# Performance work log

Measured on AMD Instinct MI355X. Metric: run time of the kernel, lower is better.

## Reference

```python
import jax, jax.numpy as jnp
import numpy as np

DELTA = 0.1
B, U_DIM, D_DIM, H_DIM, Y_DIM = 4096, 256, 64, 8192, 256
ORDER = H_DIM // 2  # 2x2 rotation blocks


def setup_inputs() -> dict:
    key = jax.random.key(0)
    k = jax.random.split(key, 6)
    u = jax.random.normal(k[0], (B, U_DIM), jnp.float32)
    du = jax.random.normal(k[1], (B, D_DIM), jnp.float32)
    h = jax.random.normal(k[2], (1, H_DIM), jnp.float32)          # h_init state
    # torch.nn.init.uniform_ -> U[0,1); +0.05 keeps 1/omega well-conditioned
    omega = jax.random.uniform(k[3], (ORDER,), jnp.float32) + 0.05
    B_w = jax.random.normal(k[4], (H_DIM, U_DIM + D_DIM), jnp.float32) / np.sqrt(U_DIM + D_DIM)
    C_w = jax.random.normal(k[5], (Y_DIM, H_DIM), jnp.float32) / np.sqrt(H_DIM)
    return {"u": u, "du": du, "h": h, "omega": omega, "B_w": B_w, "C_w": C_w}


def reference(u, du, h, omega, B_w, C_w):
    cos_t = jnp.cos(omega * DELTA)   # [order]
    sin_t = jnp.sin(omega * DELTA)   # [order]
    # exact rotation of state pairs: h viewed as [*, order, 2]
    hp = h.reshape(-1, ORDER, 2)
    h1 = cos_t * hp[..., 0] + sin_t * hp[..., 1]
    h2 = -sin_t * hp[..., 0] + cos_t * hp[..., 1]
    rec = jnp.stack([h1, h2], axis=-1).reshape(h.shape[0], -1)    # [1, h_dim]
    # input projection u_hat = B([du, u])
    udu = jnp.concatenate([du, u], axis=1)                        # [B, d+u]
    u_hat = (udu @ B_w.T).reshape(-1, ORDER, 2)                   # [B, order, 2]
    cm1 = cos_t - 1.0
    inp1 = (sin_t * u_hat[..., 0] - cm1 * u_hat[..., 1]) / omega
    inp2 = (cm1 * u_hat[..., 0] + sin_t * u_hat[..., 1]) / omega
    inp = jnp.stack([inp1, inp2], axis=-1).reshape(udu.shape[0], -1)  # [B, h_dim]
    h_new = rec + inp                                             # broadcast [B, h_dim]
    # sigma = identity, C linear readout (no bias)
    y = h_new @ C_w.T                                             # [B, y_dim]
    return y
```

## Files before the change

### kernel.cpp

```cpp
#include <hip/hip_runtime.h>
#include <hip/hip_bf16.h>

#define BN    4096
#define U_DIM 256
#define D_DIM 64
#define H_DIM 8192
#define Y_DIM 256
#define C_DIM 320
#define DELTAF 0.1f

typedef __bf16 bf16_t;
typedef __attribute__((ext_vector_type(8))) bf16_t bf16x8;
typedef __attribute__((ext_vector_type(4))) float f32x4;

__global__ __launch_bounds__(256) void gemm_E(
    const float* __restrict__ Cw, const float* __restrict__ Bw,
    const float* __restrict__ omega, const float* __restrict__ hin,
    float* __restrict__ E, float* __restrict__ y0) {
  const int b = blockIdx.x;
  const int t = threadIdx.x;
  const int wave = t >> 6, lane = t & 63;
  const int wm = wave >> 1, wn = wave & 1;
  const int l15 = lane & 15, quad = lane >> 4;

  __shared__ bf16_t lA[2][64][72];
  __shared__ bf16_t lB[2][64][72];
  __shared__ __align__(16) float cS[352], cC[352], cI[352];

  const int p = (b * 20) >> 8;
  const int bs = (256 * p + 19) / 20;
  const int P = (256 * (p + 1) + 19) / 20 - bs;
  const int c = b - bs;
  const int it0 = (c * 128) / P;
  const int it1 = ((c + 1) * 128) / P;
  const int k0 = it0 * 64;
  const int niter = it1 - it0;
  const int bm = p / 5, bn = p % 5;

  const int npairs = niter * 32;
  for (int j = t; j < npairs; j += 256) {
    const float om = omega[(k0 >> 1) + j];
    const float ang = om * DELTAF;
    cS[j] = __sinf(ang);
    cC[j] = __cosf(ang) - 1.0f;
    cI[j] = 1.0f / om;
  }
  __syncthreads();

  const int ar = t >> 2, ak = (t & 3) * 16;
  const float* gA = Cw + (size_t)(bm * 64 + ar) * H_DIM + ak;
  const float* gBb = Bw + (size_t)bn * 64 + lane;

  float4 va[4], hv[4];
  float bv[16];
  float y0acc = 0.f;

  auto gload = [&](int kk) {
#pragma unroll
    for (int q = 0; q < 4; ++q)
      va[q] = *(const float4*)(gA + kk + q * 4);
    const float* pb = gBb + (size_t)(kk + wave * 16) * C_DIM;
#pragma unroll
    for (int j = 0; j < 16; ++j) bv[j] = pb[(size_t)j * C_DIM];
    if (bn == 0) {
#pragma unroll
      for (int q = 0; q < 4; ++q)
        hv[q] = *(const float4*)(hin + kk + ak + q * 4);
    }
  };
  auto stage = [&](int kk, int buf) {
    const int jp = ((kk - k0) >> 1) + (ak >> 1);
#pragma unroll
    for (int h = 0; h < 2; ++h) {
      const float4 cs = *(const float4*)&cS[jp + h * 4];
      const float4 cc = *(const float4*)&cC[jp + h * 4];
      const float4 ci = *(const float4*)&cI[jp + h * 4];
      const float4 v0 = va[2 * h], v1 = va[2 * h + 1];
      union {
        bf16_t x[8];
        int4 v;
      } pa;
      pa.x[0] = (bf16_t)((v0.x * cs.x + v0.y * cc.x) * ci.x);
      pa.x[1] = (bf16_t)((v0.y * cs.x - v0.x * cc.x) * ci.x);
      pa.x[2] = (bf16_t)((v0.z * cs.y + v0.w * cc.y) * ci.y);
      pa.x[3] = (bf16_t)((v0.w * cs.y - v0.z * cc.y) * ci.y);
      pa.x[4] = (bf16_t)((v1.x * cs.z + v1.y * cc.z) * ci.z);
      pa.x[5] = (bf16_t)((v1.y * cs.z - v1.x * cc.z) * ci.z);
      pa.x[6] = (bf16_t)((v1.z * cs.w + v1.w * cc.w) * ci.w);
      pa.x[7] = (bf16_t)((v1.w * cs.w - v1.z * cc.w) * ci.w);
      *(int4*)&lA[buf][ar][ak + h * 8] = pa.v;
      if (bn == 0) {
        const float4 h0 = hv[2 * h], h1 = hv[2 * h + 1];
        const float c0 = cc.x + 1.f, c1 = cc.y + 1.f;
        const float c2 = cc.z + 1.f, c3 = cc.w + 1.f;
        y0acc += v0.x * (c0 * h0.x + cs.x * h0.y) +
                 v0.y * (c0 * h0.y - cs.x * h0.x) +
                 v0.z * (c1 * h0.z + cs.y * h0.w) +
                 v0.w * (c1 * h0.w - cs.y * h0.z) +
                 v1.x * (c2 * h1.x + cs.z * h1.y) +
                 v1.y * (c2 * h1.y - cs.z * h1.x) +
                 v1.z * (c3 * h1.z + cs.w * h1.w) +
                 v1.w * (c3 * h1.w - cs.w * h1.z);
      }
    }
#pragma unroll
    for (int h = 0; h < 2; ++h) {
      union {
        bf16_t x[8];
        int4 v;
      } pb;
#pragma unroll
      for (int j = 0; j < 8; ++j) pb.x[j] = (bf16_t)bv[h * 8 + j];
      *(int4*)&lB[buf][lane][wave * 16 + h * 8] = pb.v;
    }
  };

  f32x4 acc[2][2] = {};
  gload(k0);
  stage(k0, 0);
  if (niter > 1) gload(k0 + 64);
#pragma unroll 1
  for (int i = 0; i < niter; ++i) {
    __syncthreads();
    const int cur = i & 1;
#pragma unroll
    for (int kq = 0; kq < 2; ++kq) {
      const bf16x8 a0 = *(bf16x8*)&lA[cur][wm * 32 + l15][kq * 32 + quad * 8];
      const bf16x8 a1 = *(bf16x8*)&lA[cur][wm * 32 + 16 + l15][kq * 32 + quad * 8];
      const bf16x8 b0 = *(bf16x8*)&lB[cur][wn * 32 + l15][kq * 32 + quad * 8];
      const bf16x8 b1 = *(bf16x8*)&lB[cur][wn * 32 + 16 + l15][kq * 32 + quad * 8];
      acc[0][0] = __builtin_amdgcn_mfma_f32_16x16x32_bf16(a0, b0, acc[0][0], 0, 0, 0);
      acc[0][1] = __builtin_amdgcn_mfma_f32_16x16x32_bf16(a0, b1, acc[0][1], 0, 0, 0);
      acc[1][0] = __builtin_amdgcn_mfma_f32_16x16x32_bf16(a1, b0, acc[1][0], 0, 0, 0);
      acc[1][1] = __builtin_amdgcn_mfma_f32_16x16x32_bf16(a1, b1, acc[1][1], 0, 0, 0);
    }
    if (i + 1 < niter) {
      stage(k0 + (i + 1) * 64, cur ^ 1);
      if (i + 2 < niter) gload(k0 + (i + 2) * 64);
    }
  }

#pragma unroll
  for (int mt = 0; mt < 2; ++mt)
#pragma unroll
    for (int nt = 0; nt < 2; ++nt) {
      const int col = bn * 64 + wn * 32 + nt * 16 + l15;
#pragma unroll
      for (int r = 0; r < 4; ++r) {
        const int row = bm * 64 + wm * 32 + mt * 16 + quad * 4 + r;
        atomicAdd(&E[row * C_DIM + col], acc[mt][nt][r]);
      }
    }
  if (bn == 0) {
    y0acc += __shfl_xor(y0acc, 1);
    y0acc += __shfl_xor(y0acc, 2);
    if ((t & 3) == 0) atomicAdd(&y0[bm * 64 + ar], y0acc);
  }
}

__global__ __launch_bounds__(256) void gemm_Y(
    const float* __restrict__ u, const float* __restrict__ du,
    const float* __restrict__ E, const float* __restrict__ y0,
    float* __restrict__ out) {
  const int bm = blockIdx.x;
  const int bn = blockIdx.y;
  const int t = threadIdx.x;
  const int wave = t >> 6, lane = t & 63;
  const int wm = wave >> 1, wn = wave & 1;
  const int l15 = lane & 15, quad = lane >> 4;

  __shared__ bf16_t lA[2][64][72];
  __shared__ bf16_t lB[2][64][72];

  const int ar = t >> 2;
  const int ak = (t & 3) * 16;

  float4 va[4], ve[4];
  auto gload = [&](int kk) {
    const int col = kk + ak;
    const float* p = (col < D_DIM)
                         ? du + (size_t)(bm * 64 + ar) * D_DIM + col
                         : u + (size_t)(bm * 64 + ar) * U_DIM + (col - D_DIM);
#pragma unroll
    for (int q = 0; q < 4; ++q) va[q] = *(const float4*)(p + q * 4);
    const float* pe = E + (size_t)(bn * 64 + ar) * C_DIM + col;
#pragma unroll
    for (int q = 0; q < 4; ++q) ve[q] = *(const float4*)(pe + q * 4);
  };
  auto stage = [&](int buf) {
#pragma unroll
    for (int h = 0; h < 2; ++h) {
      union {
        bf16_t x[8];
        int4 v;
      } pa, pb;
      const float4 a0 = va[2 * h], a1 = va[2 * h + 1];
      const float4 e0 = ve[2 * h], e1 = ve[2 * h + 1];
      pa.x[0] = (bf16_t)a0.x; pa.x[1] = (bf16_t)a0.y;
      pa.x[2] = (bf16_t)a0.z; pa.x[3] = (bf16_t)a0.w;
      pa.x[4] = (bf16_t)a1.x; pa.x[5] = (bf16_t)a1.y;
      pa.x[6] = (bf16_t)a1.z; pa.x[7] = (bf16_t)a1.w;
      pb.x[0] = (bf16_t)e0.x; pb.x[1] = (bf16_t)e0.y;
      pb.x[2] = (bf16_t)e0.z; pb.x[3] = (bf16_t)e0.w;
      pb.x[4] = (bf16_t)e1.x; pb.x[5] = (bf16_t)e1.y;
      pb.x[6] = (bf16_t)e1.z; pb.x[7] = (bf16_t)e1.w;
      *(int4*)&lA[buf][ar][ak + h * 8] = pa.v;
      *(int4*)&lB[buf][ar][ak + h * 8] = pb.v;
    }
  };

  f32x4 acc[2][2] = {};
  gload(0);
  stage(0);
  gload(64);
#pragma unroll
  for (int i = 0; i < 5; ++i) {
    __syncthreads();
    const int cur = i & 1;
#pragma unroll
    for (int kq = 0; kq < 2; ++kq) {
      const bf16x8 a0 = *(bf16x8*)&lA[cur][wm * 32 + l15][kq * 32 + quad * 8];
      const bf16x8 a1 = *(bf16x8*)&lA[cur][wm * 32 + 16 + l15][kq * 32 + quad * 8];
      const bf16x8 b0 = *(bf16x8*)&lB[cur][wn * 32 + l15][kq * 32 + quad * 8];
      const bf16x8 b1 = *(bf16x8*)&lB[cur][wn * 32 + 16 + l15][kq * 32 + quad * 8];
      acc[0][0] = __builtin_amdgcn_mfma_f32_16x16x32_bf16(a0, b0, acc[0][0], 0, 0, 0);
      acc[0][1] = __builtin_amdgcn_mfma_f32_16x16x32_bf16(a0, b1, acc[0][1], 0, 0, 0);
      acc[1][0] = __builtin_amdgcn_mfma_f32_16x16x32_bf16(a1, b0, acc[1][0], 0, 0, 0);
      acc[1][1] = __builtin_amdgcn_mfma_f32_16x16x32_bf16(a1, b1, acc[1][1], 0, 0, 0);
    }
    if (i < 4) {
      stage(cur ^ 1);
      if (i < 3) gload((i + 2) * 64);
    }
  }
#pragma unroll
  for (int nt = 0; nt < 2; ++nt) {
    const int col = bn * 64 + wn * 32 + nt * 16 + l15;
    const float yc = y0[col];
#pragma unroll
    for (int mt = 0; mt < 2; ++mt) {
#pragma unroll
      for (int r = 0; r < 4; ++r) {
        const int row = bm * 64 + wm * 32 + mt * 16 + quad * 4 + r;
        out[(size_t)row * Y_DIM + col] = acc[mt][nt][r] + yc;
      }
    }
  }
}

extern "C" void kernel_launch(void* const* d_in, const int* in_sizes, int n_in,
                              void* d_out, int out_size, void* d_ws,
                              size_t ws_size, hipStream_t stream) {
  const float* u = (const float*)d_in[0];
  const float* du = (const float*)d_in[1];
  const float* hin = (const float*)d_in[2];
  const float* omega = (const float*)d_in[3];
  const float* Bw = (const float*)d_in[4];
  const float* Cw = (const float*)d_in[5];
  float* out = (float*)d_out;

  char* ws = (char*)d_ws;
  float* E = (float*)ws;
  float* y0 = (float*)(ws + 327680);

  gemm_E<<<256, 256, 0, stream>>>(Cw, Bw, omega, hin, E, y0);
  gemm_Y<<<dim3(BN / 64, Y_DIM / 64), 256, 0, stream>>>(u, du, E, y0, out);
}
```

Baseline: 93.89 us.

## Double K-tile in gemm_E and load all of K upfront in gemm_Y

gemm_E now uses 128-wide K tiles instead of 64, halving the per-block iteration count and the barriers, with larger shared buffers and register staging. gemm_Y drops its double-buffered K loop: each block loads the full 320-deep K slice of inputs and E into shared memory at once, syncs once, then runs all MFMAs. Both kernels get launch_bounds(256,1), letting the compiler use more registers. The cost is more LDS and register use per block, which can reduce occupancy and leaves no overlap between loads and compute in gemm_Y.

```diff
diff --git a/kernel.cpp b/kernel.cpp
--- a/kernel.cpp
+++ b/kernel.cpp
@@ -13,7 +13,7 @@
 typedef __attribute__((ext_vector_type(8))) bf16_t bf16x8;
 typedef __attribute__((ext_vector_type(4))) float f32x4;
 
-__global__ __launch_bounds__(256) void gemm_E(
+__global__ __launch_bounds__(256, 1) void gemm_E(
     const float* __restrict__ Cw, const float* __restrict__ Bw,
     const float* __restrict__ omega, const float* __restrict__ hin,
     float* __restrict__ E, float* __restrict__ y0) {
@@ -23,21 +23,21 @@
   const int wm = wave >> 1, wn = wave & 1;
   const int l15 = lane & 15, quad = lane >> 4;
 
-  __shared__ bf16_t lA[2][64][72];
-  __shared__ bf16_t lB[2][64][72];
-  __shared__ __align__(16) float cS[352], cC[352], cI[352];
+  __shared__ bf16_t lA[2][64][136];
+  __shared__ bf16_t lB[2][64][136];
+  __shared__ __align__(16) float cS[384], cC[384], cI[384];
 
   const int p = (b * 20) >> 8;
   const int bs = (256 * p + 19) / 20;
   const int P = (256 * (p + 1) + 19) / 20 - bs;
   const int c = b - bs;
-  const int it0 = (c * 128) / P;
-  const int it1 = ((c + 1) * 128) / P;
-  const int k0 = it0 * 64;
+  const int it0 = (c * 64) / P;
+  const int it1 = ((c + 1) * 64) / P;
+  const int k0 = it0 * 128;
   const int niter = it1 - it0;
   const int bm = p / 5, bn = p % 5;
 
-  const int npairs = niter * 32;
+  const int npairs = niter * 64;
   for (int j = t; j < npairs; j += 256) {
     const float om = omega[(k0 >> 1) + j];
     const float ang = om * DELTAF;
@@ -47,31 +47,31 @@
   }
   __syncthreads();
 
-  const int ar = t >> 2, ak = (t & 3) * 16;
+  const int ar = t >> 2, ak = (t & 3) * 32;
   const float* gA = Cw + (size_t)(bm * 64 + ar) * H_DIM + ak;
   const float* gBb = Bw + (size_t)bn * 64 + lane;
 
-  float4 va[4], hv[4];
-  float bv[16];
+  float4 va[8], hv[8];
+  float bv[32];
   float y0acc = 0.f;
 
   auto gload = [&](int kk) {
 #pragma unroll
-    for (int q = 0; q < 4; ++q)
+    for (int q = 0; q < 8; ++q)
       va[q] = *(const float4*)(gA + kk + q * 4);
-    const float* pb = gBb + (size_t)(kk + wave * 16) * C_DIM;
-#pragma unroll
-    for (int j = 0; j < 16; ++j) bv[j] = pb[(size_t)j * C_DIM];
+    const float* pb = gBb + (size_t)(kk + wave * 32) * C_DIM;
+#pragma unroll
+    for (int j = 0; j < 32; ++j) bv[j] = pb[(size_t)j * C_DIM];
     if (bn == 0) {
 #pragma unroll
-      for (int q = 0; q < 4; ++q)
+      for (int q = 0; q < 8; ++q)
         hv[q] = *(const float4*)(hin + kk + ak + q * 4);
     }
   };
   auto stage = [&](int kk, int buf) {
     const int jp = ((kk - k0) >> 1) + (ak >> 1);
 #pragma unroll
-    for (int h = 0; h < 2; ++h) {
+    for (int h = 0; h < 4; ++h) {
       const float4 cs = *(const float4*)&cS[jp + h * 4];
       const float4 cc = *(const float4*)&cC[jp + h * 4];
       const float4 ci = *(const float4*)&cI[jp + h * 4];
@@ -104,27 +104,27 @@
       }
     }
 #pragma unroll
-    for (int h = 0; h < 2; ++h) {
+    for (int h = 0; h < 4; ++h) {
       union {
         bf16_t x[8];
         int4 v;
       } pb;
 #pragma unroll
       for (int j = 0; j < 8; ++j) pb.x[j] = (bf16_t)bv[h * 8 + j];
-      *(int4*)&lB[buf][lane][wave * 16 + h * 8] = pb.v;
+      *(int4*)&lB[buf][lane][wave * 32 + h * 8] = pb.v;
     }
   };
 
   f32x4 acc[2][2] = {};
   gload(k0);
   stage(k0, 0);
-  if (niter > 1) gload(k0 + 64);
+  if (niter > 1) gload(k0 + 128);
 #pragma unroll 1
   for (int i = 0; i < niter; ++i) {
     __syncthreads();
     const int cur = i & 1;
 #pragma unroll
-    for (int kq = 0; kq < 2; ++kq) {
+    for (int kq = 0; kq < 4; ++kq) {
       const bf16x8 a0 = *(bf16x8*)&lA[cur][wm * 32 + l15][kq * 32 + quad * 8];
       const bf16x8 a1 = *(bf16x8*)&lA[cur][wm * 32 + 16 + l15][kq * 32 + quad * 8];
       const bf16x8 b0 = *(bf16x8*)&lB[cur][wn * 32 + l15][kq * 32 + quad * 8];
@@ -135,8 +135,8 @@
       acc[1][1] = __builtin_amdgcn_mfma_f32_16x16x32_bf16(a1, b1, acc[1][1], 0, 0, 0);
     }
     if (i + 1 < niter) {
-      stage(k0 + (i + 1) * 64, cur ^ 1);
-      if (i + 2 < niter) gload(k0 + (i + 2) * 64);
+      stage(k0 + (i + 1) * 128, cur ^ 1);
+      if (i + 2 < niter) gload(k0 + (i + 2) * 128);
     }
   }
 
@@ -158,7 +158,7 @@
   }
 }
 
-__global__ __launch_bounds__(256) void gemm_Y(
+__global__ __launch_bounds__(256, 1) void gemm_Y(
     const float* __restrict__ u, const float* __restrict__ du,
     const float* __restrict__ E, const float* __restrict__ y0,
     float* __restrict__ out) {
@@ -169,33 +169,40 @@
   const int wm = wave >> 1, wn = wave & 1;
   const int l15 = lane & 15, quad = lane >> 4;
 
-  __shared__ bf16_t lA[2][64][72];
-  __shared__ bf16_t lB[2][64][72];
+  __shared__ bf16_t lA[64][328];
+  __shared__ bf16_t lB[64][328];
 
   const int ar = t >> 2;
   const int ak = (t & 3) * 16;
 
-  float4 va[4], ve[4];
-  auto gload = [&](int kk) {
-    const int col = kk + ak;
-    const float* p = (col < D_DIM)
-                         ? du + (size_t)(bm * 64 + ar) * D_DIM + col
-                         : u + (size_t)(bm * 64 + ar) * U_DIM + (col - D_DIM);
-#pragma unroll
-    for (int q = 0; q < 4; ++q) va[q] = *(const float4*)(p + q * 4);
-    const float* pe = E + (size_t)(bn * 64 + ar) * C_DIM + col;
-#pragma unroll
-    for (int q = 0; q < 4; ++q) ve[q] = *(const float4*)(pe + q * 4);
-  };
-  auto stage = [&](int buf) {
+  float4 va[20], ve[20];
+  {
+    const float* pd = du + (size_t)(bm * 64 + ar) * D_DIM + ak;
+#pragma unroll
+    for (int q = 0; q < 4; ++q) va[q] = *(const float4*)(pd + q * 4);
+    const float* pu = u + (size_t)(bm * 64 + ar) * U_DIM + ak;
+#pragma unroll
+    for (int ck = 1; ck < 5; ++ck)
+#pragma unroll
+      for (int q = 0; q < 4; ++q)
+        va[4 * ck + q] = *(const float4*)(pu + (ck - 1) * 64 + q * 4);
+    const float* pe = E + (size_t)(bn * 64 + ar) * C_DIM + ak;
+#pragma unroll
+    for (int ck = 0; ck < 5; ++ck)
+#pragma unroll
+      for (int q = 0; q < 4; ++q)
+        ve[4 * ck + q] = *(const float4*)(pe + ck * 64 + q * 4);
+  }
+#pragma unroll
+  for (int ck = 0; ck < 5; ++ck) {
 #pragma unroll
     for (int h = 0; h < 2; ++h) {
       union {
         bf16_t x[8];
         int4 v;
       } pa, pb;
-      const float4 a0 = va[2 * h], a1 = va[2 * h + 1];
-      const float4 e0 = ve[2 * h], e1 = ve[2 * h + 1];
+      const float4 a0 = va[4 * ck + 2 * h], a1 = va[4 * ck + 2 * h + 1];
+      const float4 e0 = ve[4 * ck + 2 * h], e1 = ve[4 * ck + 2 * h + 1];
       pa.x[0] = (bf16_t)a0.x; pa.x[1] = (bf16_t)a0.y;
       pa.x[2] = (bf16_t)a0.z; pa.x[3] = (bf16_t)a0.w;
       pa.x[4] = (bf16_t)a1.x; pa.x[5] = (bf16_t)a1.y;
@@ -204,34 +211,23 @@
       pb.x[2] = (bf16_t)e0.z; pb.x[3] = (bf16_t)e0.w;
       pb.x[4] = (bf16_t)e1.x; pb.x[5] = (bf16_t)e1.y;
       pb.x[6] = (bf16_t)e1.z; pb.x[7] = (bf16_t)e1.w;
-      *(int4*)&lA[buf][ar][ak + h * 8] = pa.v;
-      *(int4*)&lB[buf][ar][ak + h * 8] = pb.v;
-    }
-  };
+      *(int4*)&lA[ar][ck * 64 + ak + h * 8] = pa.v;
+      *(int4*)&lB[ar][ck * 64 + ak + h * 8] = pb.v;
+    }
+  }
+  __syncthreads();
 
   f32x4 acc[2][2] = {};
-  gload(0);
-  stage(0);
-  gload(64);
-#pragma unroll
-  for (int i = 0; i < 5; ++i) {
-    __syncthreads();
-    const int cur = i & 1;
-#pragma unroll
-    for (int kq = 0; kq < 2; ++kq) {
-      const bf16x8 a0 = *(bf16x8*)&lA[cur][wm * 32 + l15][kq * 32 + quad * 8];
-      const bf16x8 a1 = *(bf16x8*)&lA[cur][wm * 32 + 16 + l15][kq * 32 + quad * 8];
-      const bf16x8 b0 = *(bf16x8*)&lB[cur][wn * 32 + l15][kq * 32 + quad * 8];
-      const bf16x8 b1 = *(bf16x8*)&lB[cur][wn * 32 + 16 + l15][kq * 32 + quad * 8];
-      acc[0][0] = __builtin_amdgcn_mfma_f32_16x16x32_bf16(a0, b0, acc[0][0], 0, 0, 0);
-      acc[0][1] = __builtin_amdgcn_mfma_f32_16x16x32_bf16(a0, b1, acc[0][1], 0, 0, 0);
-      acc[1][0] = __builtin_amdgcn_mfma_f32_16x16x32_bf16(a1, b0, acc[1][0], 0, 0, 0);
-      acc[1][1] = __builtin_amdgcn_mfma_f32_16x16x32_bf16(a1, b1, acc[1][1], 0, 0, 0);
-    }
-    if (i < 4) {
-      stage(cur ^ 1);
-      if (i < 3) gload((i + 2) * 64);
-    }
+#pragma unroll
+  for (int ks = 0; ks < 10; ++ks) {
+    const bf16x8 a0 = *(bf16x8*)&lA[wm * 32 + l15][ks * 32 + quad * 8];
+    const bf16x8 a1 = *(bf16x8*)&lA[wm * 32 + 16 + l15][ks * 32 + quad * 8];
+    const bf16x8 b0 = *(bf16x8*)&lB[wn * 32 + l15][ks * 32 + quad * 8];
+    const bf16x8 b1 = *(bf16x8*)&lB[wn * 32 + 16 + l15][ks * 32 + quad * 8];
+    acc[0][0] = __builtin_amdgcn_mfma_f32_16x16x32_bf16(a0, b0, acc[0][0], 0, 0, 0);
+    acc[0][1] = __builtin_amdgcn_mfma_f32_16x16x32_bf16(a0, b1, acc[0][1], 0, 0, 0);
+    acc[1][0] = __builtin_amdgcn_mfma_f32_16x16x32_bf16(a1, b0, acc[1][0], 0, 0, 0);
+    acc[1][1] = __builtin_amdgcn_mfma_f32_16x16x32_bf16(a1, b1, acc[1][1], 0, 0, 0);
   }
 #pragma unroll
   for (int nt = 0; nt < 2; ++nt) {
```

Result: slower. 95.89 us (+2.1%).
